# Kernel optimization log

Hardware: AMD Instinct MI355X
Metric: run time of the kernel (lower is better)

## Reference

```python
import jax, jax.numpy as jnp
import numpy as np

EPS = 0.01    # halting threshold eps
MU = 2.0      # halting probability multiplier
N_MAX = 16    # static upper bound on ACT steps (loop halts in 1-2 steps w/ bias=1, mu=2)

# Binarize: hard threshold at 1-eps forward, straight-through (identity) backward
@jax.custom_vjp
def binarize(x):
    return (x >= 1.0 - EPS).astype(x.dtype)

def _bin_fwd(x):
    return binarize(x), None

def _bin_bwd(_, g):
    return (g,)

binarize.defvjp(_bin_fwd, _bin_bwd)


def setup_inputs() -> dict:
    key = jax.random.key(0)
    ks = jax.random.split(key, 12)
    I, H, O = 4095, 4096, 4096
    sc = 1.0 / np.sqrt(H)
    u = lambda k, s: jax.random.uniform(k, s, jnp.float32, -sc, sc)
    return {
        "x": jax.random.normal(ks[0], (I,), jnp.float32),
        "s0": jax.random.normal(ks[1], (H,), jnp.float32) * 0.1,
        "y0": jax.random.normal(ks[2], (O,), jnp.float32),
        "h0": jnp.zeros((1,), jnp.float32),
        # nn.RNN (tanh) single layer params
        "W_ih": u(ks[3], (H, 1 + I)),
        "b_ih": u(ks[4], (H,)),
        "W_hh": u(ks[5], (H, H)),
        "b_hh": u(ks[6], (H,)),
        # fc_halt (bias hard-set to 1.0 in __init__)
        "W_halt": u(ks[7], (1, H)),
        "b_halt": jnp.ones((1,), jnp.float32),
        # fc_output
        "W_out": u(ks[8], (O, H)),
        "b_out": u(ks[9], (O,)),
    }


def reference(x, s0, y0, h0, W_ih, b_ih, W_hh, b_hh, W_halt, b_halt, W_out, b_out):
    x0 = jnp.concatenate([jnp.zeros((1,), x.dtype), x])  # skip-flag 0 input
    x1 = jnp.concatenate([jnp.ones((1,), x.dtype), x])   # skip-flag 1 input (first step)

    def step(carry, t):
        s, acc = carry
        xin = jnp.where(t == 0, x1, x0)
        valid = acc[0] < 1.0 - EPS  # ACT while-loop condition at step start
        s_new = jnp.tanh(W_ih @ xin + b_ih + W_hh @ s + b_hh)  # tanh RNN cell
        y_new = W_out @ s_new + b_out
        acc_new = acc + MU * jax.nn.sigmoid(W_halt @ s_new + b_halt)
        s_next = jnp.where(valid, s_new, s)
        acc_next = jnp.where(valid, acc_new, acc)
        return (s_next, acc_next), (s_new, y_new, acc_new, valid)

    (_, _), (S, Y, A, V) = jax.lax.scan(step, (s0, h0), jnp.arange(N_MAX))
    # S:[T,H]  Y:[T,O]  A:[T,1]  V:[T] bool
    vmask = V.astype(x.dtype)                 # steps the ACT loop actually executed
    bin_acc = binarize(A[:, 0])               # 0 before halting step, 1 at/after
    halt_bin = bin_acc * vmask                # exactly 1 at the halting step n
    h0_bin = binarize(h0)[0]
    y_sel = jnp.einsum('to,t->o', Y, halt_bin)   # torch.mv(outputs_tensor, bin)
    s_sel = jnp.einsum('th,t->h', S, halt_bin)
    output = h0_bin * y0 + (1.0 - h0_bin) * y_sel
    s = h0_bin * s0 + (1.0 - h0_bin) * s_sel
    ponder = (1.0 - h0_bin) * jnp.sum(vmask * (1.0 - bin_acc))   # = n-1, or 0 if no steps
    last_acc = h0_bin * h0 + (1.0 - h0_bin) * jnp.sum(halt_bin * A[:, 0])[None]
    return (output, s, ponder, last_acc - 1.0)
```

## Files before the change

kernel.cpp:

```cpp
#include <hip/hip_runtime.h>
#include <math.h>


#define H      4096
#define NMAX   16
#define THRESH 0.99f

__device__ __forceinline__ float wave_reduce(float a) {
    #pragma unroll
    for (int off = 32; off > 0; off >>= 1) a += __shfl_down(a, off);
    return a;
}

__global__ __launch_bounds__(256) void k_prep(
    const float* __restrict__ x, float* __restrict__ ws, float* __restrict__ out)
{
    const int i = blockIdx.x * 256 + threadIdx.x;
    if (i < 32) ws[i] = 0.f;
    if (i == 0) out[2048] = 0.f;
    if (i < H - 1) out[2048 + 1 + i] = x[i];
}

__global__ __launch_bounds__(256, 8) void k_step0(
    const float* __restrict__ s0,     const float* __restrict__ h0,
    const float* __restrict__ W_ih,   const float* __restrict__ b_ih,
    const float* __restrict__ W_hh,   const float* __restrict__ b_hh,
    const float* __restrict__ W_halt,
    float* __restrict__ ws, float* __restrict__ out)
{
    if (h0[0] >= THRESH) return;

    const int tid  = threadIdx.x, bid = blockIdx.x;
    const int wave = tid >> 6,   lane = tid & 63;
    const int row  = bid * 2 + (wave >> 1);
    const int half = wave & 1;

    const float4* wih = (const float4*)(W_ih + (size_t)row * H);
    const float4* whh = (const float4*)(W_hh + (size_t)row * H);
    const float4* xv  = (const float4*)(out + 2048);
    const float4* sv  = (const float4*)s0;

    const int base = half * 512 + lane;
    float a0 = 0.f, a1 = 0.f;
    #pragma unroll
    for (int k = 0; k < 8; ++k) {
        const int idx = base + (k << 6);
        float4 w0 = wih[idx], v0 = xv[idx];
        float4 w1 = whh[idx], v1 = sv[idx];
        a0 += w0.x*v0.x + w0.y*v0.y + w0.z*v0.z + w0.w*v0.w;
        a1 += w1.x*v1.x + w1.y*v1.y + w1.z*v1.z + w1.w*v1.w;
    }
    float a = wave_reduce(a0 + a1);

    __shared__ float part[4];
    if (lane == 0) part[wave] = a;
    __syncthreads();
    if (tid == 0) {
        const int r0 = bid * 2, r1 = r0 + 1;
        float z0 = part[0] + part[1] + b_ih[r0] + b_hh[r0] + W_ih[(size_t)r0 * H];
        float z1 = part[2] + part[3] + b_ih[r1] + b_hh[r1] + W_ih[(size_t)r1 * H];
        float s1a = tanhf(z0), s1b = tanhf(z1);
        ws[32 + r0] = s1a;
        ws[32 + r1] = s1b;
        out[bid] = W_halt[r0] * s1a + W_halt[r1] * s1b;
    }
}

__global__ __launch_bounds__(256) void k_halt(
    const float* __restrict__ h0, const float* __restrict__ b_halt,
    const float* __restrict__ hp, float* ws)
{
    if (h0[0] >= THRESH) return;
    const int tid = threadIdx.x;
    const float4* h4 = (const float4*)hp;
    float a = 0.f;
    for (int i = tid; i < 512; i += 256) { float4 v = h4[i]; a += v.x + v.y + v.z + v.w; }
    a = wave_reduce(a);
    __shared__ float part[4];
    if ((tid & 63) == 0) part[tid >> 6] = a;
    __syncthreads();
    if (tid == 0) {
        float hd  = part[0] + part[1] + part[2] + part[3];
        float sg  = 1.f / (1.f + expf(-(hd + b_halt[0])));
        float acc = h0[0] + 2.f * sg;
        int*  wsI = (int*)ws;
        int halted = (acc >= THRESH) ? 1 : 0;
        wsI[4] = halted;
        wsI[5] = 0;
        wsI[6] = halted ? 0 : 1;
        ws[7]  = acc;
        ws[8]  = acc;
    }
}

#define RG   256
#define RT   256

__device__ __forceinline__ void grid_barrier(int* cnt, int* gen) {
    __syncthreads();
    if (threadIdx.x == 0) {
        __threadfence();
        int g = __hip_atomic_load(gen, __ATOMIC_RELAXED, __HIP_MEMORY_SCOPE_AGENT);
        int prev = __hip_atomic_fetch_add(cnt, 1, __ATOMIC_ACQ_REL, __HIP_MEMORY_SCOPE_AGENT);
        if (prev == RG - 1) {
            __hip_atomic_store(cnt, 0, __ATOMIC_RELAXED, __HIP_MEMORY_SCOPE_AGENT);
            __hip_atomic_fetch_add(gen, 1, __ATOMIC_RELEASE, __HIP_MEMORY_SCOPE_AGENT);
        } else {
            while (__hip_atomic_load(gen, __ATOMIC_ACQUIRE, __HIP_MEMORY_SCOPE_AGENT) == g)
                __builtin_amdgcn_s_sleep(8);
        }
        __threadfence();
    }
    __syncthreads();
}

__global__ __launch_bounds__(RT) void k_rest(
    const float* __restrict__ x,
    const float* __restrict__ h0,
    const float* __restrict__ W_ih,   const float* __restrict__ b_ih,
    const float* __restrict__ W_hh,   const float* __restrict__ b_hh,
    const float* __restrict__ W_halt, const float* __restrict__ b_halt,
    float* ws)
{
    int* wsI = (int*)ws;
    if (h0[0] >= THRESH) return;
    if (wsI[4]) return;

    float* hdot = ws + 16;
    float* sb0  = ws + 32;
    float* sb1  = ws + 32 + H;

    const int tid = threadIdx.x, bid = blockIdx.x;
    const int wave = tid >> 6, lane = tid & 63;

    __shared__ float xl[H];
    __shared__ float sl[H];
    if (tid == 0) xl[0] = 0.f;
    for (int i = tid; i < H - 1; i += RT) xl[i + 1] = x[i];

    float acc    = ws[7];
    int   ponder = wsI[6];
    const float bh = b_halt[0];
    bool  halted = false;
    int   sel = 0;
    float last_acc = 0.f;

    for (int t = 1; t < NMAX; ++t) {
        const float* scur = (t & 1) ? sb0 : sb1;
        float*       snew = (t & 1) ? sb1 : sb0;

        __syncthreads();
        for (int i = tid; i < H / 4; i += RT)
            ((float4*)sl)[i] = ((const float4*)scur)[i];
        __syncthreads();

        for (int r = 0; r < 4; ++r) {
            const int row = bid * 16 + r * 4 + wave;
            const float4* wih = (const float4*)(W_ih + (size_t)row * H);
            const float4* whh = (const float4*)(W_hh + (size_t)row * H);
            float a0 = 0.f, a1 = 0.f;
            #pragma unroll 4
            for (int k = 0; k < 16; ++k) {
                const int idx = lane + (k << 6);
                float4 wa = wih[idx], wb = whh[idx];
                float4 va = ((const float4*)xl)[idx], vb = ((const float4*)sl)[idx];
                a0 += wa.x*va.x + wa.y*va.y + wa.z*va.z + wa.w*va.w;
                a1 += wb.x*vb.x + wb.y*vb.y + wb.z*vb.z + wb.w*vb.w;
            }
            float a = wave_reduce(a0 + a1);
            if (lane == 0) {
                float sv = tanhf(a + b_ih[row] + b_hh[row]);
                snew[row] = sv;
                atomicAdd(&hdot[t], W_halt[row] * sv);
            }
        }

        grid_barrier((int*)ws, (int*)ws + 1);

        float hd = ((volatile float*)hdot)[t];
        float sg = 1.f / (1.f + expf(-(hd + bh)));
        acc += 2.f * sg;
        if (acc >= THRESH) { halted = true; last_acc = acc; sel = (t & 1) ? 1 : 0; break; }
        ponder++;
    }

    if (bid == 0 && tid == 0) {
        wsI[4] = halted ? 1 : 0;
        wsI[5] = sel;
        wsI[6] = ponder;
        ws[8]  = last_acc;
    }
}

__global__ __launch_bounds__(256, 8) void k_out(
    const float* __restrict__ s0,    const float* __restrict__ y0,
    const float* __restrict__ h0,
    const float* __restrict__ W_out, const float* __restrict__ b_out,
    const float* __restrict__ ws, float* __restrict__ out)
{
    const float h0v = h0[0];
    const int tid = threadIdx.x, bid = blockIdx.x;

    if (h0v >= THRESH) {
        for (int i = bid * 256 + tid; i < H; i += 2048 * 256) {
            out[i]     = y0[i];
            out[H + i] = s0[i];
        }
        if (bid == 0 && tid == 0) { out[2*H] = 0.f; out[2*H + 1] = h0v - 1.f; }
        return;
    }

    const int* wsI = (const int*)ws;
    if (!wsI[4]) {
        for (int i = bid * 256 + tid; i < H; i += 2048 * 256) {
            out[i]     = 0.f;
            out[H + i] = 0.f;
        }
        if (bid == 0 && tid == 0) { out[2*H] = (float)wsI[6]; out[2*H + 1] = -1.f; }
        return;
    }

    const float* sfin = ws + 32 + (wsI[5] ? H : 0);
    const int wave = tid >> 6, lane = tid & 63;
    const int row  = bid * 2 + (wave >> 1);
    const int half = wave & 1;

    const float4* wo = (const float4*)(W_out + (size_t)row * H);
    const float4* sv = (const float4*)sfin;
    const int base = half * 512 + lane;
    float a0 = 0.f, a1 = 0.f;
    #pragma unroll
    for (int k = 0; k < 8; k += 2) {
        const int i0 = base + (k << 6), i1 = base + ((k + 1) << 6);
        float4 w0 = wo[i0], v0 = sv[i0];
        float4 w1 = wo[i1], v1 = sv[i1];
        a0 += w0.x*v0.x + w0.y*v0.y + w0.z*v0.z + w0.w*v0.w;
        a1 += w1.x*v1.x + w1.y*v1.y + w1.z*v1.z + w1.w*v1.w;
    }
    float a = wave_reduce(a0 + a1);

    __shared__ float part[4];
    if (lane == 0) part[wave] = a;
    __syncthreads();
    if (tid == 0) {
        const int r0 = bid * 2, r1 = r0 + 1;
        out[r0]     = part[0] + part[1] + b_out[r0];
        out[r1]     = part[2] + part[3] + b_out[r1];
        out[H + r0] = sfin[r0];
        out[H + r1] = sfin[r1];
        if (bid == 0) {
            out[2*H]     = (float)wsI[6];
            out[2*H + 1] = ws[8] - 1.f;
        }
    }
}

extern "C" void kernel_launch(void* const* d_in, const int* in_sizes, int n_in,
                              void* d_out, int out_size, void* d_ws, size_t ws_size,
                              hipStream_t stream) {
    const float* x      = (const float*)d_in[0];
    const float* s0     = (const float*)d_in[1];
    const float* y0     = (const float*)d_in[2];
    const float* h0     = (const float*)d_in[3];
    const float* W_ih   = (const float*)d_in[4];
    const float* b_ih   = (const float*)d_in[5];
    const float* W_hh   = (const float*)d_in[6];
    const float* b_hh   = (const float*)d_in[7];
    const float* W_halt = (const float*)d_in[8];
    const float* b_halt = (const float*)d_in[9];
    const float* W_out  = (const float*)d_in[10];
    const float* b_out  = (const float*)d_in[11];
    float* out = (float*)d_out;
    float* ws  = (float*)d_ws;

    k_prep<<<dim3(16),   dim3(256), 0, stream>>>(x, ws, out);
    k_step0<<<dim3(2048), dim3(256), 0, stream>>>(
        s0, h0, W_ih, b_ih, W_hh, b_hh, W_halt, ws, out);
    k_halt<<<dim3(1),    dim3(256), 0, stream>>>(h0, b_halt, out, ws);
    k_rest<<<dim3(RG),   dim3(RT),  0, stream>>>(
        x, h0, W_ih, b_ih, W_hh, b_hh, W_halt, b_halt, ws);
    k_out<<<dim3(2048),  dim3(256), 0, stream>>>(
        s0, y0, h0, W_out, b_out, ws, out);
}
```

Baseline: 231.4 us.

## Assign one row per wave with LDS-staged vectors and register-prefetched weights

```diff
diff --git a/kernel.cpp b/kernel.cpp
--- a/kernel.cpp
+++ b/kernel.cpp
@@ -21,7 +21,8 @@
     if (i < H - 1) out[2048 + 1 + i] = x[i];
 }
 
-__global__ __launch_bounds__(256, 8) void k_step0(
+#define P0 4
+__global__ __launch_bounds__(256, 4) void k_step0(
     const float* __restrict__ s0,     const float* __restrict__ h0,
     const float* __restrict__ W_ih,   const float* __restrict__ b_ih,
     const float* __restrict__ W_hh,   const float* __restrict__ b_hh,
@@ -32,38 +33,59 @@
 
     const int tid  = threadIdx.x, bid = blockIdx.x;
     const int wave = tid >> 6,   lane = tid & 63;
-    const int row  = bid * 2 + (wave >> 1);
-    const int half = wave & 1;
-
+
+    __shared__ float xl[H];
+    __shared__ float sl[H];
+    {
+        const float4* xg = (const float4*)(out + 2048);
+        const float4* sg = (const float4*)s0;
+        #pragma unroll
+        for (int i = 0; i < 4; ++i) {
+            ((float4*)xl)[tid + (i << 8)] = xg[tid + (i << 8)];
+            ((float4*)sl)[tid + (i << 8)] = sg[tid + (i << 8)];
+        }
+    }
+    __syncthreads();
+
+    const int row = bid * 4 + wave;
     const float4* wih = (const float4*)(W_ih + (size_t)row * H);
     const float4* whh = (const float4*)(W_hh + (size_t)row * H);
-    const float4* xv  = (const float4*)(out + 2048);
-    const float4* sv  = (const float4*)s0;
-
-    const int base = half * 512 + lane;
-    float a0 = 0.f, a1 = 0.f;
-    #pragma unroll
-    for (int k = 0; k < 8; ++k) {
-        const int idx = base + (k << 6);
-        float4 w0 = wih[idx], v0 = xv[idx];
-        float4 w1 = whh[idx], v1 = sv[idx];
-        a0 += w0.x*v0.x + w0.y*v0.y + w0.z*v0.z + w0.w*v0.w;
-        a1 += w1.x*v1.x + w1.y*v1.y + w1.z*v1.z + w1.w*v1.w;
-    }
-    float a = wave_reduce(a0 + a1);
-
-    __shared__ float part[4];
-    if (lane == 0) part[wave] = a;
-    __syncthreads();
-    if (tid == 0) {
-        const int r0 = bid * 2, r1 = r0 + 1;
-        float z0 = part[0] + part[1] + b_ih[r0] + b_hh[r0] + W_ih[(size_t)r0 * H];
-        float z1 = part[2] + part[3] + b_ih[r1] + b_hh[r1] + W_ih[(size_t)r1 * H];
-        float s1a = tanhf(z0), s1b = tanhf(z1);
-        ws[32 + r0] = s1a;
-        ws[32 + r1] = s1b;
-        out[bid] = W_halt[r0] * s1a + W_halt[r1] * s1b;
-    }
+    const float4* xv  = (const float4*)xl;
+    const float4* sv  = (const float4*)sl;
+
+    float4 wa[P0], wb[P0];
+    #pragma unroll
+    for (int p = 0; p < P0; ++p) {
+        wa[p] = wih[lane + (p << 6)];
+        wb[p] = whh[lane + (p << 6)];
+    }
+    float a0 = 0.f, a1 = 0.f, a2 = 0.f, a3 = 0.f;
+    #pragma unroll
+    for (int k = 0; k < 16; ++k) {
+        const int s = k & (P0 - 1);
+        float4 cwa = wa[s], cwb = wb[s];
+        const int kp = k + P0;
+        if (kp < 16) {
+            wa[s] = wih[lane + (kp << 6)];
+            wb[s] = whh[lane + (kp << 6)];
+        }
+        float4 va = xv[lane + (k << 6)], vb = sv[lane + (k << 6)];
+        a0 += cwa.x*va.x + cwa.y*va.y;
+        a1 += cwa.z*va.z + cwa.w*va.w;
+        a2 += cwb.x*vb.x + cwb.y*vb.y;
+        a3 += cwb.z*vb.z + cwb.w*vb.w;
+    }
+    float a = wave_reduce((a0 + a1) + (a2 + a3));
+
+    __shared__ float hp[4];
+    if (lane == 0) {
+        float z  = a + b_ih[row] + b_hh[row] + W_ih[(size_t)row * H];
+        float s1 = tanhf(z);
+        ws[32 + row] = s1;
+        hp[wave] = W_halt[row] * s1;
+    }
+    __syncthreads();
+    if (tid == 0) out[bid] = hp[0] + hp[1] + hp[2] + hp[3];
 }
 
 __global__ __launch_bounds__(256) void k_halt(
@@ -73,9 +95,8 @@
     if (h0[0] >= THRESH) return;
     const int tid = threadIdx.x;
     const float4* h4 = (const float4*)hp;
-    float a = 0.f;
-    for (int i = tid; i < 512; i += 256) { float4 v = h4[i]; a += v.x + v.y + v.z + v.w; }
-    a = wave_reduce(a);
+    float4 v = h4[tid];
+    float a = wave_reduce(v.x + v.y + v.z + v.w);
     __shared__ float part[4];
     if ((tid & 63) == 0) part[tid >> 6] = a;
     __syncthreads();
@@ -192,7 +213,8 @@
     }
 }
 
-__global__ __launch_bounds__(256, 8) void k_out(
+#define P1 6
+__global__ __launch_bounds__(256, 4) void k_out(
     const float* __restrict__ s0,    const float* __restrict__ y0,
     const float* __restrict__ h0,
     const float* __restrict__ W_out, const float* __restrict__ b_out,
@@ -202,7 +224,7 @@
     const int tid = threadIdx.x, bid = blockIdx.x;
 
     if (h0v >= THRESH) {
-        for (int i = bid * 256 + tid; i < H; i += 2048 * 256) {
+        for (int i = bid * 256 + tid; i < H; i += 1024 * 256) {
             out[i]     = y0[i];
             out[H + i] = s0[i];
         }
@@ -212,7 +234,7 @@
 
     const int* wsI = (const int*)ws;
     if (!wsI[4]) {
-        for (int i = bid * 256 + tid; i < H; i += 2048 * 256) {
+        for (int i = bid * 256 + tid; i < H; i += 1024 * 256) {
             out[i]     = 0.f;
             out[H + i] = 0.f;
         }
@@ -221,37 +243,42 @@
     }
 
     const float* sfin = ws + 32 + (wsI[5] ? H : 0);
+    __shared__ float sl[H];
+    {
+        const float4* sg = (const float4*)sfin;
+        #pragma unroll
+        for (int i = 0; i < 4; ++i)
+            ((float4*)sl)[tid + (i << 8)] = sg[tid + (i << 8)];
+    }
+    __syncthreads();
+
     const int wave = tid >> 6, lane = tid & 63;
-    const int row  = bid * 2 + (wave >> 1);
-    const int half = wave & 1;
-
+    const int row  = bid * 4 + wave;
     const float4* wo = (const float4*)(W_out + (size_t)row * H);
-    const float4* sv = (const float4*)sfin;
-    const int base = half * 512 + lane;
+    const float4* sv = (const float4*)sl;
+
+    float4 w[P1];
+    #pragma unroll
+    for (int p = 0; p < P1; ++p) w[p] = wo[lane + (p << 6)];
     float a0 = 0.f, a1 = 0.f;
     #pragma unroll
-    for (int k = 0; k < 8; k += 2) {
-        const int i0 = base + (k << 6), i1 = base + ((k + 1) << 6);
-        float4 w0 = wo[i0], v0 = sv[i0];
-        float4 w1 = wo[i1], v1 = sv[i1];
-        a0 += w0.x*v0.x + w0.y*v0.y + w0.z*v0.z + w0.w*v0.w;
-        a1 += w1.x*v1.x + w1.y*v1.y + w1.z*v1.z + w1.w*v1.w;
+    for (int k = 0; k < 16; ++k) {
+        const int s = k % P1;
+        float4 cw = w[s];
+        const int kp = k + P1;
+        if (kp < 16) w[s] = wo[lane + (kp << 6)];
+        float4 v = sv[lane + (k << 6)];
+        a0 += cw.x*v.x + cw.y*v.y;
+        a1 += cw.z*v.z + cw.w*v.w;
     }
     float a = wave_reduce(a0 + a1);
-
-    __shared__ float part[4];
-    if (lane == 0) part[wave] = a;
-    __syncthreads();
-    if (tid == 0) {
-        const int r0 = bid * 2, r1 = r0 + 1;
-        out[r0]     = part[0] + part[1] + b_out[r0];
-        out[r1]     = part[2] + part[3] + b_out[r1];
-        out[H + r0] = sfin[r0];
-        out[H + r1] = sfin[r1];
-        if (bid == 0) {
-            out[2*H]     = (float)wsI[6];
-            out[2*H + 1] = ws[8] - 1.f;
-        }
+    if (lane == 0) {
+        out[row]     = a + b_out[row];
+        out[H + row] = sl[row];
+    }
+    if (bid == 0 && tid == 0) {
+        out[2*H]     = (float)wsI[6];
+        out[2*H + 1] = ws[8] - 1.f;
     }
 }
 
@@ -274,11 +301,11 @@
     float* ws  = (float*)d_ws;
 
     k_prep<<<dim3(16),   dim3(256), 0, stream>>>(x, ws, out);
-    k_step0<<<dim3(2048), dim3(256), 0, stream>>>(
+    k_step0<<<dim3(1024), dim3(256), 0, stream>>>(
         s0, h0, W_ih, b_ih, W_hh, b_hh, W_halt, ws, out);
     k_halt<<<dim3(1),    dim3(256), 0, stream>>>(h0, b_halt, out, ws);
     k_rest<<<dim3(RG),   dim3(RT),  0, stream>>>(
         x, h0, W_ih, b_ih, W_hh, b_hh, W_halt, b_halt, ws);
-    k_out<<<dim3(2048),  dim3(256), 0, stream>>>(
+    k_out<<<dim3(1024),  dim3(256), 0, stream>>>(
         s0, y0, h0, W_out, b_out, ws, out);
 }
```

Measured after the change: 224.4 us. 3.0% less time.

## Fold halt reduction into recurrent kernel and widen matvec blocks to one row each

Applied to the files above, without the earlier changes.

```diff
diff --git a/kernel.cpp b/kernel.cpp
--- a/kernel.cpp
+++ b/kernel.cpp
@@ -17,11 +17,11 @@
 {
     const int i = blockIdx.x * 256 + threadIdx.x;
     if (i < 32) ws[i] = 0.f;
-    if (i == 0) out[2048] = 0.f;
-    if (i < H - 1) out[2048 + 1 + i] = x[i];
-}
-
-__global__ __launch_bounds__(256, 8) void k_step0(
+    if (i == 0) out[H] = 0.f;
+    if (i < H - 1) out[H + 1 + i] = x[i];
+}
+
+__global__ __launch_bounds__(512, 4) void k_step0(
     const float* __restrict__ s0,     const float* __restrict__ h0,
     const float* __restrict__ W_ih,   const float* __restrict__ b_ih,
     const float* __restrict__ W_hh,   const float* __restrict__ b_hh,
@@ -32,64 +32,34 @@
 
     const int tid  = threadIdx.x, bid = blockIdx.x;
     const int wave = tid >> 6,   lane = tid & 63;
-    const int row  = bid * 2 + (wave >> 1);
-    const int half = wave & 1;
-
-    const float4* wih = (const float4*)(W_ih + (size_t)row * H);
-    const float4* whh = (const float4*)(W_hh + (size_t)row * H);
-    const float4* xv  = (const float4*)(out + 2048);
-    const float4* sv  = (const float4*)s0;
-
-    const int base = half * 512 + lane;
-    float a0 = 0.f, a1 = 0.f;
-    #pragma unroll
-    for (int k = 0; k < 8; ++k) {
-        const int idx = base + (k << 6);
-        float4 w0 = wih[idx], v0 = xv[idx];
-        float4 w1 = whh[idx], v1 = sv[idx];
-        a0 += w0.x*v0.x + w0.y*v0.y + w0.z*v0.z + w0.w*v0.w;
-        a1 += w1.x*v1.x + w1.y*v1.y + w1.z*v1.z + w1.w*v1.w;
-    }
+    const int q    = wave & 3,   m    = wave >> 2;
+    const int row  = bid;
+
+    const float4* w4 = (const float4*)((m ? W_hh : W_ih) + (size_t)row * H);
+    const float4* v4 = (const float4*)(m ? s0 : (out + H));
+    const int base = q * 256 + lane;
+
+    float4 w0 = w4[base      ], w1 = w4[base +  64],
+           w2 = w4[base + 128], w3 = w4[base + 192];
+    float4 v0 = v4[base      ], v1 = v4[base +  64],
+           v2 = v4[base + 128], v3 = v4[base + 192];
+
+    float a0 = w0.x*v0.x + w0.y*v0.y + w0.z*v0.z + w0.w*v0.w
+             + w2.x*v2.x + w2.y*v2.y + w2.z*v2.z + w2.w*v2.w;
+    float a1 = w1.x*v1.x + w1.y*v1.y + w1.z*v1.z + w1.w*v1.w
+             + w3.x*v3.x + w3.y*v3.y + w3.z*v3.z + w3.w*v3.w;
     float a = wave_reduce(a0 + a1);
 
-    __shared__ float part[4];
+    __shared__ float part[8];
     if (lane == 0) part[wave] = a;
     __syncthreads();
     if (tid == 0) {
-        const int r0 = bid * 2, r1 = r0 + 1;
-        float z0 = part[0] + part[1] + b_ih[r0] + b_hh[r0] + W_ih[(size_t)r0 * H];
-        float z1 = part[2] + part[3] + b_ih[r1] + b_hh[r1] + W_ih[(size_t)r1 * H];
-        float s1a = tanhf(z0), s1b = tanhf(z1);
-        ws[32 + r0] = s1a;
-        ws[32 + r1] = s1b;
-        out[bid] = W_halt[r0] * s1a + W_halt[r1] * s1b;
-    }
-}
-
-__global__ __launch_bounds__(256) void k_halt(
-    const float* __restrict__ h0, const float* __restrict__ b_halt,
-    const float* __restrict__ hp, float* ws)
-{
-    if (h0[0] >= THRESH) return;
-    const int tid = threadIdx.x;
-    const float4* h4 = (const float4*)hp;
-    float a = 0.f;
-    for (int i = tid; i < 512; i += 256) { float4 v = h4[i]; a += v.x + v.y + v.z + v.w; }
-    a = wave_reduce(a);
-    __shared__ float part[4];
-    if ((tid & 63) == 0) part[tid >> 6] = a;
-    __syncthreads();
-    if (tid == 0) {
-        float hd  = part[0] + part[1] + part[2] + part[3];
-        float sg  = 1.f / (1.f + expf(-(hd + b_halt[0])));
-        float acc = h0[0] + 2.f * sg;
-        int*  wsI = (int*)ws;
-        int halted = (acc >= THRESH) ? 1 : 0;
-        wsI[4] = halted;
-        wsI[5] = 0;
-        wsI[6] = halted ? 0 : 1;
-        ws[7]  = acc;
-        ws[8]  = acc;
+        float z = part[0] + part[1] + part[2] + part[3]
+                + part[4] + part[5] + part[6] + part[7]
+                + b_ih[row] + b_hh[row] + W_ih[(size_t)row * H];
+        float s1 = tanhf(z);
+        ws[32 + row] = s1;
+        out[row] = W_halt[row] * s1;
     }
 }
 
@@ -120,26 +90,67 @@
     const float* __restrict__ W_ih,   const float* __restrict__ b_ih,
     const float* __restrict__ W_hh,   const float* __restrict__ b_hh,
     const float* __restrict__ W_halt, const float* __restrict__ b_halt,
-    float* ws)
+    const float* __restrict__ hpart,  float* ws)
 {
     int* wsI = (int*)ws;
     if (h0[0] >= THRESH) return;
-    if (wsI[4]) return;
+
+    const int tid = threadIdx.x, bid = blockIdx.x;
+    const int wave = tid >> 6, lane = tid & 63;
+
+    {
+        const float4* p4 = (const float4*)hpart;
+        float a = 0.f;
+        #pragma unroll
+        for (int j = 0; j < 4; ++j) {
+            float4 v = p4[tid + (j << 8)];
+            a += v.x + v.y + v.z + v.w;
+        }
+        a = wave_reduce(a);
+        __shared__ float pr[4];
+        if (lane == 0) pr[wave] = a;
+        __syncthreads();
+        float hd  = pr[0] + pr[1] + pr[2] + pr[3];
+        float sg  = 1.f / (1.f + expf(-(hd + b_halt[0])));
+        float acc0 = h0[0] + 2.f * sg;
+        if (acc0 >= THRESH) {
+            if (bid == 0 && tid == 0) {
+                wsI[4] = 1; wsI[5] = 0; wsI[6] = 0; ws[8] = acc0;
+            }
+            return;
+        }
+        if (bid == 0 && tid == 0) { wsI[4] = 0; }
+        __syncthreads();
+        pr[0] = acc0;
+        __syncthreads();
+    }
 
     float* hdot = ws + 16;
     float* sb0  = ws + 32;
     float* sb1  = ws + 32 + H;
-
-    const int tid = threadIdx.x, bid = blockIdx.x;
-    const int wave = tid >> 6, lane = tid & 63;
 
     __shared__ float xl[H];
     __shared__ float sl[H];
     if (tid == 0) xl[0] = 0.f;
     for (int i = tid; i < H - 1; i += RT) xl[i + 1] = x[i];
 
-    float acc    = ws[7];
-    int   ponder = wsI[6];
+    float acc;
+    {
+        const float4* p4 = (const float4*)hpart;
+        float a = 0.f;
+        #pragma unroll
+        for (int j = 0; j < 4; ++j) {
+            float4 v = p4[tid + (j << 8)];
+            a += v.x + v.y + v.z + v.w;
+        }
+        a = wave_reduce(a);
+        __shared__ float pr2[4];
+        if (lane == 0) pr2[wave] = a;
+        __syncthreads();
+        float hd = pr2[0] + pr2[1] + pr2[2] + pr2[3];
+        acc = h0[0] + 2.f / (1.f + expf(-(hd + b_halt[0])));
+    }
+    int   ponder = 1;
     const float bh = b_halt[0];
     bool  halted = false;
     int   sel = 0;
@@ -192,7 +203,7 @@
     }
 }
 
-__global__ __launch_bounds__(256, 8) void k_out(
+__global__ __launch_bounds__(512, 4) void k_out(
     const float* __restrict__ s0,    const float* __restrict__ y0,
     const float* __restrict__ h0,
     const float* __restrict__ W_out, const float* __restrict__ b_out,
@@ -202,50 +213,47 @@
     const int tid = threadIdx.x, bid = blockIdx.x;
 
     if (h0v >= THRESH) {
-        for (int i = bid * 256 + tid; i < H; i += 2048 * 256) {
-            out[i]     = y0[i];
-            out[H + i] = s0[i];
-        }
-        if (bid == 0 && tid == 0) { out[2*H] = 0.f; out[2*H + 1] = h0v - 1.f; }
+        const int i = bid * 512 + tid;
+        if (i < H) { out[i] = y0[i]; out[H + i] = s0[i]; }
+        if (i == 0) { out[2*H] = 0.f; out[2*H + 1] = h0v - 1.f; }
         return;
     }
 
     const int* wsI = (const int*)ws;
     if (!wsI[4]) {
-        for (int i = bid * 256 + tid; i < H; i += 2048 * 256) {
-            out[i]     = 0.f;
-            out[H + i] = 0.f;
-        }
-        if (bid == 0 && tid == 0) { out[2*H] = (float)wsI[6]; out[2*H + 1] = -1.f; }
+        const int i = bid * 512 + tid;
+        if (i < H) { out[i] = 0.f; out[H + i] = 0.f; }
+        if (i == 0) { out[2*H] = (float)wsI[6]; out[2*H + 1] = -1.f; }
         return;
     }
 
     const float* sfin = ws + 32 + (wsI[5] ? H : 0);
     const int wave = tid >> 6, lane = tid & 63;
-    const int row  = bid * 2 + (wave >> 1);
-    const int half = wave & 1;
-
-    const float4* wo = (const float4*)(W_out + (size_t)row * H);
-    const float4* sv = (const float4*)sfin;
-    const int base = half * 512 + lane;
-    float a0 = 0.f, a1 = 0.f;
-    #pragma unroll
-    for (int k = 0; k < 8; k += 2) {
-        const int i0 = base + (k << 6), i1 = base + ((k + 1) << 6);
-        float4 w0 = wo[i0], v0 = sv[i0];
-        float4 w1 = wo[i1], v1 = sv[i1];
-        a0 += w0.x*v0.x + w0.y*v0.y + w0.z*v0.z + w0.w*v0.w;
-        a1 += w1.x*v1.x + w1.y*v1.y + w1.z*v1.z + w1.w*v1.w;
-    }
+    const int row  = bid * 2 + (wave >> 2);
+    const int q    = wave & 3;
+
+    const float4* w4 = (const float4*)(W_out + (size_t)row * H);
+    const float4* v4 = (const float4*)sfin;
+    const int base = q * 256 + lane;
+
+    float4 w0 = w4[base      ], w1 = w4[base +  64],
+           w2 = w4[base + 128], w3 = w4[base + 192];
+    float4 v0 = v4[base      ], v1 = v4[base +  64],
+           v2 = v4[base + 128], v3 = v4[base + 192];
+
+    float a0 = w0.x*v0.x + w0.y*v0.y + w0.z*v0.z + w0.w*v0.w
+             + w2.x*v2.x + w2.y*v2.y + w2.z*v2.z + w2.w*v2.w;
+    float a1 = w1.x*v1.x + w1.y*v1.y + w1.z*v1.z + w1.w*v1.w
+             + w3.x*v3.x + w3.y*v3.y + w3.z*v3.z + w3.w*v3.w;
     float a = wave_reduce(a0 + a1);
 
-    __shared__ float part[4];
+    __shared__ float part[8];
     if (lane == 0) part[wave] = a;
     __syncthreads();
     if (tid == 0) {
         const int r0 = bid * 2, r1 = r0 + 1;
-        out[r0]     = part[0] + part[1] + b_out[r0];
-        out[r1]     = part[2] + part[3] + b_out[r1];
+        out[r0]     = part[0] + part[1] + part[2] + part[3] + b_out[r0];
+        out[r1]     = part[4] + part[5] + part[6] + part[7] + b_out[r1];
         out[H + r0] = sfin[r0];
         out[H + r1] = sfin[r1];
         if (bid == 0) {
@@ -274,11 +282,10 @@
     float* ws  = (float*)d_ws;
 
     k_prep<<<dim3(16),   dim3(256), 0, stream>>>(x, ws, out);
-    k_step0<<<dim3(2048), dim3(256), 0, stream>>>(
+    k_step0<<<dim3(4096), dim3(512), 0, stream>>>(
         s0, h0, W_ih, b_ih, W_hh, b_hh, W_halt, ws, out);
-    k_halt<<<dim3(1),    dim3(256), 0, stream>>>(h0, b_halt, out, ws);
     k_rest<<<dim3(RG),   dim3(RT),  0, stream>>>(
-        x, h0, W_ih, b_ih, W_hh, b_hh, W_halt, b_halt, ws);
-    k_out<<<dim3(2048),  dim3(256), 0, stream>>>(
+        x, h0, W_ih, b_ih, W_hh, b_hh, W_halt, b_halt, out, ws);
+    k_out<<<dim3(2048),  dim3(512), 0, stream>>>(
         s0, y0, h0, W_out, b_out, ws, out);
 }
```

Result: faster. 217.0 us (-6.2%).
